# Performance work log

Measured on AMD Instinct MI355X. Metric: run time of the kernel, lower is better.

## Reference

```python
import jax, jax.numpy as jnp
import numpy as np

N = 50000   # nodes
E = 500000  # edges
G = 64      # graphs in batch
H = 2       # attention heads
D = 64      # hidden per head (hid)
F_IN = 4    # num_features
C = 5       # num_classes
NEG_SLOPE = 0.2


def setup_inputs() -> dict:
    key = jax.random.key(0)
    ks = jax.random.split(key, 24)
    inp = {
        'x': jax.random.normal(ks[0], (N, F_IN), jnp.float32),
        'edge_index': jax.random.randint(ks[1], (2, E), 0, N, dtype=jnp.int64),
        'batch': jnp.sort(jax.random.randint(ks[2], (N,), 0, G, dtype=jnp.int64)),
    }
    ins = [F_IN, H * D, H * D, H * D]
    ki = 3
    for l, fin in enumerate(ins, 1):
        s = 1.0 / np.sqrt(fin)
        inp[f'W{l}'] = s * jax.random.normal(ks[ki], (fin, H * D), jnp.float32); ki += 1
        inp[f'asrc{l}'] = 0.1 * jax.random.normal(ks[ki], (H, D), jnp.float32); ki += 1
        inp[f'adst{l}'] = 0.1 * jax.random.normal(ks[ki], (H, D), jnp.float32); ki += 1
        inp[f'b{l}'] = 0.01 * jax.random.normal(ks[ki], (H * D,), jnp.float32); ki += 1
    inp['lin_w'] = (1.0 / np.sqrt(H * D)) * jax.random.normal(ks[ki], (H * D, C), jnp.float32); ki += 1
    inp['lin_b'] = jnp.zeros((C,), jnp.float32)
    return inp


def gat_conv(x, src, dst, W, a_src, a_dst, b):
    # x: [N, Fin] -> h: [N, H, D]
    h = (x @ W).reshape(-1, H, D)
    alpha_src = jnp.sum(h * a_src, axis=-1)  # [N, H]
    alpha_dst = jnp.sum(h * a_dst, axis=-1)  # [N, H]
    e = jax.nn.leaky_relu(alpha_src[src] + alpha_dst[dst], NEG_SLOPE)  # [E, H]
    # segment softmax over incoming edges of each dst node
    e_max = jax.ops.segment_max(e, dst, num_segments=N)  # [N, H]
    e_exp = jnp.exp(e - e_max[dst])
    denom = jax.ops.segment_sum(e_exp, dst, num_segments=N)
    alpha = e_exp / (denom[dst] + 1e-16)  # [E, H]
    msg = h[src] * alpha[:, :, None]  # [E, H, D]
    out = jax.ops.segment_sum(msg, dst, num_segments=N)  # [N, H, D]
    return out.reshape(-1, H * D) + b


def reference(x, edge_index, batch,
              W1, asrc1, adst1, b1,
              W2, asrc2, adst2, b2,
              W3, asrc3, adst3, b3,
              W4, asrc4, adst4, b4,
              lin_w, lin_b):
    src, dst = edge_index[0], edge_index[1]
    h = jax.nn.relu(gat_conv(x, src, dst, W1, asrc1, adst1, b1))
    h = jax.nn.relu(gat_conv(h, src, dst, W2, asrc2, adst2, b2))
    h = jax.nn.relu(gat_conv(h, src, dst, W3, asrc3, adst3, b3))
    h = jax.nn.relu(gat_conv(h, src, dst, W4, asrc4, adst4, b4))
    # global mean pool over graphs
    sums = jax.ops.segment_sum(h, batch, num_segments=G)  # [G, 128]
    counts = jax.ops.segment_sum(jnp.ones((h.shape[0],), h.dtype), batch, num_segments=G)
    pooled = sums / jnp.maximum(counts, 1.0)[:, None]
    return jax.nn.sigmoid(pooled @ lin_w + lin_b)  # [G, C]
```

## Files before the change

### kernel.cpp

```cpp
#include <hip/hip_runtime.h>
#include <math.h>

#define NHEAD 2
#define NDIM  64
#define HD    128
#define NGRAPH 64
#define NCLS  5
#define NEG_SLOPE 0.2f
#define LDA 136

typedef __attribute__((ext_vector_type(8))) short bf16x8;
typedef __attribute__((ext_vector_type(4))) float f32x4;

static __device__ __forceinline__ unsigned short f2bf(float f) {
    unsigned int u = __float_as_uint(f);
    u = (u + 0x7fff + ((u >> 16) & 1)) >> 16;
    return (unsigned short)u;
}
static __device__ __forceinline__ float bf2f(unsigned short b) {
    return __uint_as_float((unsigned int)b << 16);
}


__global__ void k_deg(const int* __restrict__ dst, int* __restrict__ deg, int E) {
    int i = blockIdx.x * blockDim.x + threadIdx.x;
    if (i < E) atomicAdd(&deg[dst[i]], 1);
}

__global__ __launch_bounds__(256) void k_scan_local(const int* __restrict__ deg,
                                                    int* __restrict__ ptr,
                                                    int* __restrict__ bsum, int n) {
    __shared__ int wsum[4];
    const int tid = threadIdx.x, lane = tid & 63, wid = tid >> 6;
    const int base = blockIdx.x * 2048 + tid * 8;
    int v[8];
    #pragma unroll
    for (int k = 0; k < 8; ++k) {
        int i = base + k;
        v[k] = (i < n) ? deg[i] : 0;
    }
    #pragma unroll
    for (int k = 1; k < 8; ++k) v[k] += v[k - 1];
    int x = v[7];
    #pragma unroll
    for (int off = 1; off < 64; off <<= 1) {
        int t = __shfl_up(x, off, 64);
        if (lane >= off) x += t;
    }
    if (lane == 63) wsum[wid] = x;
    __syncthreads();
    int woff = 0;
    #pragma unroll
    for (int k = 0; k < 4; ++k) woff += (k < wid) ? wsum[k] : 0;
    int texcl = woff + x - v[7];
    #pragma unroll
    for (int k = 0; k < 8; ++k) {
        int i = base + k;
        if (i < n) ptr[i + 1] = texcl + v[k];
    }
    if (tid == 255) bsum[blockIdx.x] = woff + x;
    if (blockIdx.x == 0 && tid == 0) ptr[0] = 0;
}

__global__ void k_scan_bsum(int* __restrict__ bsum, int B) {
    int lane = threadIdx.x;
    int carry = 0;
    for (int base = 0; base < B; base += 64) {
        int i = base + lane;
        int v = (i < B) ? bsum[i] : 0;
        int x = v;
        #pragma unroll
        for (int off = 1; off < 64; off <<= 1) {
            int t = __shfl_up(x, off, 64);
            if (lane >= off) x += t;
        }
        if (i < B) bsum[i] = carry + x - v;
        carry += __shfl(x, 63, 64);
    }
}

__global__ __launch_bounds__(256) void k_scan_add(int* __restrict__ ptr,
                                                  const int* __restrict__ bsum, int n) {
    int off = bsum[blockIdx.x];
    if (off == 0) return;
    const int base = blockIdx.x * 2048 + threadIdx.x * 8;
    #pragma unroll
    for (int k = 0; k < 8; ++k) {
        int i = base + k;
        if (i < n) ptr[i + 1] += off;
    }
}

__global__ void k_scatter(const int* __restrict__ src, const int* __restrict__ dst,
                          const int* __restrict__ ptr, int* __restrict__ fill,
                          int* __restrict__ csr, int E) {
    int i = blockIdx.x * blockDim.x + threadIdx.x;
    if (i < E) {
        int d = dst[i];
        int pos = atomicAdd(&fill[d], 1);
        csr[ptr[d] + pos] = src[i];
    }
}


__global__ void k_prepw(const float* __restrict__ W2, const float* __restrict__ W3,
                        const float* __restrict__ W4, unsigned short* __restrict__ Wt) {
    int idx = blockIdx.x * blockDim.x + threadIdx.x;
    if (idx >= 3 * HD * HD) return;
    int l = idx / (HD * HD), rem = idx % (HD * HD);
    int n = rem >> 7, k = rem & 127;
    const float* W = (l == 0) ? W2 : (l == 1) ? W3 : W4;
    Wt[idx] = f2bf(W[k * HD + n]);
}

__global__ void k_gemm1_alpha(const float* __restrict__ x, const float* __restrict__ W,
                              const float* __restrict__ asrc, const float* __restrict__ adst,
                              unsigned short* __restrict__ out, float* __restrict__ oas,
                              float* __restrict__ oad, int N) {
    int n = (blockIdx.x * blockDim.x + threadIdx.x) >> 6;
    int lane = threadIdx.x & 63;
    if (n >= N) return;
    float4 xv = *(const float4*)&x[n * 4];
    int c0 = lane * 2;
    float2 w0 = *(const float2*)&W[c0];
    float2 w1 = *(const float2*)&W[128 + c0];
    float2 w2 = *(const float2*)&W[256 + c0];
    float2 w3 = *(const float2*)&W[384 + c0];
    float v0 = xv.x * w0.x + xv.y * w1.x + xv.z * w2.x + xv.w * w3.x;
    float v1 = xv.x * w0.y + xv.y * w1.y + xv.z * w2.y + xv.w * w3.y;
    unsigned short b0 = f2bf(v0), b1 = f2bf(v1);
    unsigned int packed = (unsigned int)b0 | ((unsigned int)b1 << 16);
    *(unsigned int*)&out[(size_t)n * HD + c0] = packed;
    float vx = bf2f(b0), vy = bf2f(b1);
    float2 av = *(const float2*)&asrc[c0];
    float2 dv = *(const float2*)&adst[c0];
    float s = vx * av.x + vy * av.y;
    float t = vx * dv.x + vy * dv.y;
    #pragma unroll
    for (int off = 16; off > 0; off >>= 1) {
        s += __shfl_xor(s, off);
        t += __shfl_xor(t, off);
    }
    if ((lane & 31) == 0) {
        int head = lane >> 5;
        oas[n * 2 + head] = s;
        oad[n * 2 + head] = t;
    }
}

static __device__ __forceinline__ void agg_acc(
    const unsigned short* __restrict__ h, const float* __restrict__ oas,
    const float* __restrict__ oad,
    const int* __restrict__ ptr, const int* __restrict__ csr,
    int n, int N, int sub, int hsel, float* acc, float& denom) {
    #pragma unroll
    for (int k = 0; k < 8; ++k) acc[k] = 0.f;
    denom = 0.f;
    if (n >= N) return;
    const int beg = ptr[n], end = ptr[n + 1];
    const float adh = oad[n * 2 + hsel];

    auto weight = [&](float as) {
        float e = as + adh;
        e = (e >= 0.f) ? e : NEG_SLOPE * e;
        e = fminf(e, 80.f);
        return __expf(e);
    };
    auto accum = [&](uint4 hv, float a) {
        denom += a;
        #pragma unroll
        for (int k = 0; k < 4; ++k) {
            unsigned int u = (&hv.x)[k];
            acc[2 * k]     += a * __uint_as_float(u << 16);
            acc[2 * k + 1] += a * __uint_as_float(u & 0xffff0000u);
        }
    };

    int j = beg;
    for (; j + 4 <= end; j += 4) {
        int s0 = csr[j], s1 = csr[j + 1], s2 = csr[j + 2], s3 = csr[j + 3];
        uint4 h0 = *(const uint4*)&h[(size_t)s0 * HD + sub * 8];
        uint4 h1 = *(const uint4*)&h[(size_t)s1 * HD + sub * 8];
        uint4 h2 = *(const uint4*)&h[(size_t)s2 * HD + sub * 8];
        uint4 h3 = *(const uint4*)&h[(size_t)s3 * HD + sub * 8];
        float x0 = oas[s0 * 2 + hsel], x1 = oas[s1 * 2 + hsel];
        float x2 = oas[s2 * 2 + hsel], x3 = oas[s3 * 2 + hsel];
        accum(h0, weight(x0));
        accum(h1, weight(x1));
        accum(h2, weight(x2));
        accum(h3, weight(x3));
    }
    for (; j < end; ++j) {
        int s = csr[j];
        uint4 hv = *(const uint4*)&h[(size_t)s * HD + sub * 8];
        float xs = oas[s * 2 + hsel];
        accum(hv, weight(xs));
    }
}

static __device__ __forceinline__ uint4 norm_bias_relu_pack(
    const float* acc, float denom, const float* __restrict__ bias, int sub) {
    float inv = 1.f / (denom + 1e-16f);
    float4 ba = *(const float4*)&bias[sub * 8];
    float4 bb = *(const float4*)&bias[sub * 8 + 4];
    float o[8];
    o[0] = fmaxf(acc[0] * inv + ba.x, 0.f);
    o[1] = fmaxf(acc[1] * inv + ba.y, 0.f);
    o[2] = fmaxf(acc[2] * inv + ba.z, 0.f);
    o[3] = fmaxf(acc[3] * inv + ba.w, 0.f);
    o[4] = fmaxf(acc[4] * inv + bb.x, 0.f);
    o[5] = fmaxf(acc[5] * inv + bb.y, 0.f);
    o[6] = fmaxf(acc[6] * inv + bb.z, 0.f);
    o[7] = fmaxf(acc[7] * inv + bb.w, 0.f);
    uint4 pk;
    pk.x = (unsigned int)f2bf(o[0]) | ((unsigned int)f2bf(o[1]) << 16);
    pk.y = (unsigned int)f2bf(o[2]) | ((unsigned int)f2bf(o[3]) << 16);
    pk.z = (unsigned int)f2bf(o[4]) | ((unsigned int)f2bf(o[5]) << 16);
    pk.w = (unsigned int)f2bf(o[6]) | ((unsigned int)f2bf(o[7]) << 16);
    return pk;
}

__global__ __launch_bounds__(256, 8) void k_agg_gemm(
    const unsigned short* __restrict__ hin,
    const float* __restrict__ oas_in, const float* __restrict__ oad_in,
    const int* __restrict__ ptr, const int* __restrict__ csr,
    const float* __restrict__ bias,
    const unsigned short* __restrict__ Wt,
    const float* __restrict__ asrc, const float* __restrict__ adst,
    unsigned short* __restrict__ hout,
    float* __restrict__ oas_out, float* __restrict__ oad_out, int N) {
    __shared__ unsigned short As[16 * LDA];
    __shared__ unsigned short Ot[16][HD];
    __shared__ float psL[4][16], pdL[4][16];
    const int tid = threadIdx.x;
    const int lane = tid & 63, w = tid >> 6;
    const int grp = lane >> 4, sub = lane & 15;
    const int hsel = sub >> 3;
    const int nbase = blockIdx.x * 16;

    const int row = w * 4 + grp;
    float acc8[8], denom;
    agg_acc(hin, oas_in, oad_in, ptr, csr, nbase + row, N, sub, hsel, acc8, denom);
    uint4 pk = norm_bias_relu_pack(acc8, denom, bias, sub);
    *(uint4*)&As[(size_t)row * LDA + sub * 8] = pk;
    __syncthreads();

    float av2[2], dv2[2];
    #pragma unroll
    for (int i = 0; i < 2; ++i) {
        int c = w * 2 + i;
        av2[i] = asrc[c * 16 + sub];
        dv2[i] = adst[c * 16 + sub];
    }
    f32x4 acc[2];
    acc[0] = (f32x4)(0.f);
    acc[1] = (f32x4)(0.f);
    #pragma unroll
    for (int ks = 0; ks < 4; ++ks) {
        bf16x8 a0 = *(const bf16x8*)&As[(size_t)sub * LDA + ks * 32 + grp * 8];
        #pragma unroll
        for (int i = 0; i < 2; ++i) {
            int c = w * 2 + i;
            bf16x8 b = *(const bf16x8*)&Wt[(size_t)(c * 16 + sub) * HD + ks * 32 + grp * 8];
            acc[i] = __builtin_amdgcn_mfma_f32_16x16x32_bf16(a0, b, acc[i], 0, 0, 0);
        }
    }

    #pragma unroll
    for (int i = 0; i < 2; ++i) {
        int col = (w * 2 + i) * 16 + sub;
        #pragma unroll
        for (int r = 0; r < 4; ++r)
            Ot[grp * 4 + r][col] = f2bf(acc[i][r]);
    }
    #pragma unroll
    for (int r = 0; r < 4; ++r) {
        float ps = acc[0][r] * av2[0] + acc[1][r] * av2[1];
        float pd = acc[0][r] * dv2[0] + acc[1][r] * dv2[1];
        #pragma unroll
        for (int off = 1; off < 16; off <<= 1) {
            ps += __shfl_xor(ps, off);
            pd += __shfl_xor(pd, off);
        }
        if (sub == 0) {
            psL[w][grp * 4 + r] = ps;
            pdL[w][grp * 4 + r] = pd;
        }
    }
    __syncthreads();

    {
        int r2 = tid >> 4, c16 = tid & 15;
        int gn = nbase + r2;
        if (gn < N) {
            uint4 v = *(const uint4*)&Ot[r2][c16 * 8];
            *(uint4*)&hout[(size_t)gn * HD + c16 * 8] = v;
        }
    }
    if (tid < 32) {
        int r2 = tid & 15, head = tid >> 4;
        int n2 = nbase + r2;
        if (n2 < N) {
            float s = psL[2 * head][r2] + psL[2 * head + 1][r2];
            float d = pdL[2 * head][r2] + pdL[2 * head + 1][r2];
            oas_out[n2 * 2 + head] = s;
            oad_out[n2 * 2 + head] = d;
        }
    }
}

__global__ __launch_bounds__(256) void k_agg_final(
    const unsigned short* __restrict__ hin,
    const float* __restrict__ oas_in, const float* __restrict__ oad_in,
    const int* __restrict__ ptr, const int* __restrict__ csr,
    const float* __restrict__ bias,
    unsigned short* __restrict__ out, int N) {
    const int tid = threadIdx.x;
    const int lane = tid & 63;
    const int grp = lane >> 4, sub = lane & 15;
    const int hsel = sub >> 3;
    const int n = ((blockIdx.x * blockDim.x + tid) >> 6) * 4 + grp;
    float acc8[8], denom;
    agg_acc(hin, oas_in, oad_in, ptr, csr, n, N, sub, hsel, acc8, denom);
    if (n < N) {
        uint4 pk = norm_bias_relu_pack(acc8, denom, bias, sub);
        *(uint4*)&out[(size_t)n * HD + sub * 8] = pk;
    }
}

__global__ void k_pool(const unsigned short* __restrict__ feat, const int* __restrict__ batch,
                       float* __restrict__ pooled, int* __restrict__ gcount, int N) {
    int col = threadIdx.x;
    int n0 = blockIdx.x * 128;
    int n1 = min(n0 + 128, N);
    float acc = 0.f;
    int curg = -1, runlen = 0;
    for (int n = n0; n < n1; ++n) {
        int g = batch[n];
        if (g != curg) {
            if (curg >= 0) {
                atomicAdd(&pooled[curg * HD + col], acc);
                if (col == 0) atomicAdd(&gcount[curg], runlen);
            }
            acc = 0.f; runlen = 0;
            curg = g;
        }
        acc += bf2f(feat[(size_t)n * HD + col]);
        runlen++;
    }
    if (curg >= 0) {
        atomicAdd(&pooled[curg * HD + col], acc);
        if (col == 0) atomicAdd(&gcount[curg], runlen);
    }
}

__global__ void k_final(const float* __restrict__ pooled, const int* __restrict__ gcount,
                        const float* __restrict__ lw, const float* __restrict__ lb,
                        float* __restrict__ out) {
    int tid = threadIdx.x;
    if (tid >= NGRAPH * NCLS) return;
    int g = tid / NCLS, c = tid % NCLS;
    float cnt = fmaxf((float)gcount[g], 1.f);
    const float* p = pooled + g * HD;
    float sum = 0.f;
    for (int k = 0; k < HD; ++k)
        sum += p[k] * lw[k * NCLS + c];
    float z = lb[c] + sum / cnt;
    out[tid] = 1.f / (1.f + __expf(-z));
}


static inline size_t al256(size_t x) { return (x + 255) & ~(size_t)255; }

extern "C" void kernel_launch(void* const* d_in, const int* in_sizes, int n_in,
                              void* d_out, int out_size, void* d_ws, size_t ws_size,
                              hipStream_t stream) {
    const int N = in_sizes[0] / 4;
    const int E = in_sizes[1] / 2;

    const float* x     = (const float*)d_in[0];
    const int*   esrc  = (const int*)d_in[1];
    const int*   edst  = esrc + E;
    const int*   batch = (const int*)d_in[2];
    const float* Wl[4]  = {(const float*)d_in[3],  (const float*)d_in[7],
                           (const float*)d_in[11], (const float*)d_in[15]};
    const float* asr[4] = {(const float*)d_in[4],  (const float*)d_in[8],
                           (const float*)d_in[12], (const float*)d_in[16]};
    const float* ads[4] = {(const float*)d_in[5],  (const float*)d_in[9],
                           (const float*)d_in[13], (const float*)d_in[17]};
    const float* bs[4]  = {(const float*)d_in[6],  (const float*)d_in[10],
                           (const float*)d_in[14], (const float*)d_in[18]};
    const float* lin_w = (const float*)d_in[19];
    const float* lin_b = (const float*)d_in[20];
    float* out = (float*)d_out;

    char* w = (char*)d_ws;
    size_t off = 0;
    auto alloc = [&](size_t bytes) -> void* {
        void* p = w + off;
        off = al256(off + bytes);
        return p;
    };
    int*   deg    = (int*)alloc((size_t)N * 4);
    int*   fill   = (int*)alloc((size_t)N * 4);
    int*   gcount = (int*)alloc((size_t)NGRAPH * 4);
    float* pooled = (float*)alloc((size_t)NGRAPH * HD * 4);
    size_t zbytes = off;
    int*   ptr    = (int*)alloc((size_t)(N + 1) * 4);
    int*   bsum   = (int*)alloc((size_t)1024 * 4);
    int*   csr    = (int*)alloc((size_t)E * 4);
    unsigned short* hA   = (unsigned short*)alloc((size_t)N * HD * 2);
    unsigned short* hB   = (unsigned short*)alloc((size_t)N * HD * 2);
    unsigned short* feat = (unsigned short*)alloc((size_t)N * HD * 2);
    unsigned short* Wt   = (unsigned short*)alloc((size_t)3 * HD * HD * 2);
    float* asA = (float*)alloc((size_t)N * 2 * 4);
    float* adA = (float*)alloc((size_t)N * 2 * 4);
    float* asB = (float*)alloc((size_t)N * 2 * 4);
    float* adB = (float*)alloc((size_t)N * 2 * 4);
    (void)ws_size; (void)n_in; (void)out_size;

    hipMemsetAsync(d_ws, 0, zbytes, stream);

    k_prepw<<<(3 * HD * HD + 255) / 256, 256, 0, stream>>>(Wl[1], Wl[2], Wl[3], Wt);
    k_deg<<<(E + 255) / 256, 256, 0, stream>>>(edst, deg, E);
    const int SB = (N + 2047) / 2048;
    k_scan_local<<<SB, 256, 0, stream>>>(deg, ptr, bsum, N);
    k_scan_bsum<<<1, 64, 0, stream>>>(bsum, SB);
    k_scan_add<<<SB, 256, 0, stream>>>(ptr, bsum, N);
    k_scatter<<<(E + 255) / 256, 256, 0, stream>>>(esrc, edst, ptr, fill, csr, E);

    const int fblk = (N + 15) / 16;

    k_gemm1_alpha<<<(N + 3) / 4, 256, 0, stream>>>(
        x, Wl[0], asr[0], ads[0], hA, asA, adA, N);

    const unsigned short* hc = hA; unsigned short* hn = hB;
    const float* cas = asA; const float* cad = adA;
    float* nas = asB;       float* nad = adB;
    for (int i = 0; i < 4; ++i) {
        if (i < 3) {
            k_agg_gemm<<<fblk, 256, 0, stream>>>(
                hc, cas, cad, ptr, csr, bs[i],
                Wt + (size_t)i * HD * HD, asr[i + 1], ads[i + 1],
                hn, nas, nad, N);
            const unsigned short* th = hc; hc = hn; hn = (unsigned short*)th;
            const float* ts = cas; cas = nas; nas = (float*)ts;
            const float* td = cad; cad = nad; nad = (float*)td;
        } else {
            k_agg_final<<<fblk, 256, 0, stream>>>(
                hc, cas, cad, ptr, csr, bs[i], feat, N);
        }
    }

    k_pool<<<(N + 127) / 128, 128, 0, stream>>>(feat, batch, pooled, gcount, N);
    k_final<<<1, 320, 0, stream>>>(pooled, gcount, lin_w, lin_b, out);
}
```

Baseline: 337.9 us.

## Sort CSR neighbors by source range buckets for gather locality

Builds the CSR with each destination's incoming edges grouped into 8 source-index buckets, so neighbor gathers across the aggregation touch sources in a coarsely sorted order. The degree, scan and scatter stages now operate over N*8 segments instead of N. The aim is better cache locality in the feature gathers of each layer, at the cost of a larger scan and more memset and atomic traffic in preprocessing. k_scan_bsum is launched as a single 64-thread block over SB block sums; with NSEG the count SB grows to about 196, and whether that kernel handles it is not visible.

```diff
diff --git a/kernel.cpp b/kernel.cpp
--- a/kernel.cpp
+++ b/kernel.cpp
@@ -8,6 +8,7 @@
 #define NCLS  5
 #define NEG_SLOPE 0.2f
 #define LDA 136
+#define NRANGE 8
 
 typedef __attribute__((ext_vector_type(8))) short bf16x8;
 typedef __attribute__((ext_vector_type(4))) float f32x4;
@@ -22,9 +23,13 @@
 }
 
 
-__global__ void k_deg(const int* __restrict__ dst, int* __restrict__ deg, int E) {
+__global__ void k_deg(const int* __restrict__ src, const int* __restrict__ dst,
+                      int* __restrict__ deg, int E, int Rsz) {
     int i = blockIdx.x * blockDim.x + threadIdx.x;
-    if (i < E) atomicAdd(&deg[dst[i]], 1);
+    if (i < E) {
+        int r = src[i] / Rsz;
+        atomicAdd(&deg[(size_t)dst[i] * NRANGE + r], 1);
+    }
 }
 
 __global__ __launch_bounds__(256) void k_scan_local(const int* __restrict__ deg,
@@ -93,12 +98,13 @@
 
 __global__ void k_scatter(const int* __restrict__ src, const int* __restrict__ dst,
                           const int* __restrict__ ptr, int* __restrict__ fill,
-                          int* __restrict__ csr, int E) {
+                          int* __restrict__ csr, int E, int Rsz) {
     int i = blockIdx.x * blockDim.x + threadIdx.x;
     if (i < E) {
-        int d = dst[i];
-        int pos = atomicAdd(&fill[d], 1);
-        csr[ptr[d] + pos] = src[i];
+        int s = src[i];
+        int seg = dst[i] * NRANGE + s / Rsz;
+        int pos = atomicAdd(&fill[seg], 1);
+        csr[ptr[seg] + pos] = s;
     }
 }
 
@@ -157,7 +163,7 @@
     for (int k = 0; k < 8; ++k) acc[k] = 0.f;
     denom = 0.f;
     if (n >= N) return;
-    const int beg = ptr[n], end = ptr[n + 1];
+    const int beg = ptr[n * NRANGE], end = ptr[n * NRANGE + NRANGE];
     const float adh = oad[n * 2 + hsel];
 
     auto weight = [&](float as) {
@@ -377,6 +383,8 @@
                               hipStream_t stream) {
     const int N = in_sizes[0] / 4;
     const int E = in_sizes[1] / 2;
+    const int Rsz = (N + NRANGE - 1) / NRANGE;
+    const int NSEG = N * NRANGE;
 
     const float* x     = (const float*)d_in[0];
     const int*   esrc  = (const int*)d_in[1];
@@ -401,12 +409,12 @@
         off = al256(off + bytes);
         return p;
     };
-    int*   deg    = (int*)alloc((size_t)N * 4);
-    int*   fill   = (int*)alloc((size_t)N * 4);
+    int*   deg    = (int*)alloc((size_t)NSEG * 4);
+    int*   fill   = (int*)alloc((size_t)NSEG * 4);
     int*   gcount = (int*)alloc((size_t)NGRAPH * 4);
     float* pooled = (float*)alloc((size_t)NGRAPH * HD * 4);
     size_t zbytes = off;
-    int*   ptr    = (int*)alloc((size_t)(N + 1) * 4);
+    int*   ptr    = (int*)alloc((size_t)(NSEG + 1) * 4);
     int*   bsum   = (int*)alloc((size_t)1024 * 4);
     int*   csr    = (int*)alloc((size_t)E * 4);
     unsigned short* hA   = (unsigned short*)alloc((size_t)N * HD * 2);
@@ -422,12 +430,12 @@
     hipMemsetAsync(d_ws, 0, zbytes, stream);
 
     k_prepw<<<(3 * HD * HD + 255) / 256, 256, 0, stream>>>(Wl[1], Wl[2], Wl[3], Wt);
-    k_deg<<<(E + 255) / 256, 256, 0, stream>>>(edst, deg, E);
-    const int SB = (N + 2047) / 2048;
-    k_scan_local<<<SB, 256, 0, stream>>>(deg, ptr, bsum, N);
+    k_deg<<<(E + 255) / 256, 256, 0, stream>>>(esrc, edst, deg, E, Rsz);
+    const int SB = (NSEG + 2047) / 2048;
+    k_scan_local<<<SB, 256, 0, stream>>>(deg, ptr, bsum, NSEG);
     k_scan_bsum<<<1, 64, 0, stream>>>(bsum, SB);
-    k_scan_add<<<SB, 256, 0, stream>>>(ptr, bsum, N);
-    k_scatter<<<(E + 255) / 256, 256, 0, stream>>>(esrc, edst, ptr, fill, csr, E);
+    k_scan_add<<<SB, 256, 0, stream>>>(ptr, bsum, NSEG);
+    k_scatter<<<(E + 255) / 256, 256, 0, stream>>>(esrc, edst, ptr, fill, csr, E, Rsz);
 
     const int fblk = (N + 15) / 16;
 
```

Result: no change. 337.2 us (-0.2%).
